# Performance work log

Hardware: AMD Instinct MI355X
Metric: run time of the kernel (lower is better)

## Reference

```python
import jax, jax.numpy as jnp
import numpy as np


def setup_inputs() -> dict:
    key = jax.random.key(0)
    k1, k2 = jax.random.split(key)
    B, D, H, W, K = 64, 256, 32, 32, 1024
    x = jax.random.normal(k1, (B, D, H, W), dtype=jnp.float32)
    # codebook: torch.rand -> uniform [0,1), shape (emb_dim, num_emb)
    emb = jax.random.uniform(k2, (D, K), dtype=jnp.float32)
    return {"x": x, "emb": emb}


def reference(x, emb):
    # x: (B, D, H, W); emb: (D, K)
    B, D, H, W = x.shape
    K = emb.shape[1]
    # flatten latents: (N, D) with N = B*H*W (matches permute(0,2,3,1).view)
    xf = x.transpose(0, 2, 3, 1).reshape(-1, D)
    # (argmin of squared dist == argmin of L2 norm in the torch code)
    d2 = (
        jnp.sum(xf * xf, axis=1, keepdims=True)
        - 2.0 * (xf @ emb)
        + jnp.sum(emb * emb, axis=0)[None, :]
    )  # (N, K)
    argmin = jnp.argmin(d2, axis=1)  # (N,)
    q = jnp.take(emb.T, argmin, axis=0)  # (N, D) gather of nearest codes
    out = q.reshape(B, H, W, D).transpose(0, 3, 1, 2)  # back to (B, D, H, W)
    return out, argmin.reshape(B, H, W)
```

## Files before the change

kernel.cpp:

```cpp
#include <hip/hip_runtime.h>


typedef _Float16 half8 __attribute__((ext_vector_type(8)));
typedef float f32x4v __attribute__((ext_vector_type(4)));
typedef float f32x16 __attribute__((ext_vector_type(16)));
typedef const __attribute__((address_space(1))) unsigned int* gp_t;
typedef __attribute__((address_space(3))) unsigned int* lp_t;

#define K_DIM 1024
#define D_DIM 256

__global__ __launch_bounds__(256) void vq_prep(const float* __restrict__ emb,
                                               float* __restrict__ nhp,
                                               char* __restrict__ eimg_h,
                                               char* __restrict__ eimg_l) {
  __shared__ float tile[32][66];
  const int t = threadIdx.x;
  const int ki = blockIdx.x >> 3, di = blockIdx.x & 7;
  const int d0 = di * 32, k0 = ki * 64;
#pragma unroll
  for (int r = 0; r < 4; ++r) {
    int slot = r * 256 + t;
    int dr = slot >> 5, c2 = slot & 31;
    float2 v = *(const float2*)(emb + (size_t)(d0 + dr) * K_DIM + k0 + c2 * 2);
    *(float2*)&tile[dr][c2 * 2] = v;
  }
  __syncthreads();
  const int codeL = t >> 2, q = t & 3;
  half8 hh, ll;
  float s = 0.f;
#pragma unroll
  for (int j = 0; j < 8; ++j) {
    float v = tile[q * 8 + j][codeL];
    _Float16 h = (_Float16)v;
    hh[j] = h;
    ll[j] = (_Float16)(v - (float)h);
    s = fmaf(v, v, s);
  }
  const int dblk = di * 4 + q;
  const int phys = dblk ^ (codeL & 31);
  const size_t off = (size_t)ki * 32768 + codeL * 512 + phys * 16;
  *(half8*)(eimg_h + off) = hh;
  *(half8*)(eimg_l + off) = ll;
  s += __shfl_xor(s, 1);
  s += __shfl_xor(s, 2);
  if (q == 0) nhp[di * K_DIM + k0 + codeL] = s;
}

#define STAGE(tile_i, bufsel)                                                \
  {                                                                          \
    const size_t tb = (size_t)(tile_i) * 32768 + w * 1024 + l * 16;          \
    _Pragma("unroll") for (int r = 0; r < 8; ++r) {                          \
      __builtin_amdgcn_global_load_lds((gp_t)(eimg_h + tb + r * 4096),       \
                                       (lp_t)(ebuf_h[bufsel] + w * 1024 +    \
                                              r * 4096),                     \
                                       16, 0, 0);                            \
      __builtin_amdgcn_global_load_lds((gp_t)(eimg_l + tb + r * 4096),       \
                                       (lp_t)(ebuf_l[bufsel] + w * 1024 +    \
                                              r * 4096),                     \
                                       16, 0, 0);                            \
    }                                                                        \
  }

__global__ __launch_bounds__(256, 1) void vq_main(
    const float* __restrict__ x, const float* __restrict__ emb,
    const float* __restrict__ nhp, const char* __restrict__ eimg_h,
    const char* __restrict__ eimg_l, float* __restrict__ out,
    float* __restrict__ aout) {
  __shared__ __align__(16) char ebuf_h[2][32768];
  __shared__ __align__(16) char ebuf_l[2][32768];
  __shared__ __align__(16) float x_lds[16][256];
  __shared__ float nh_s[1024];
  __shared__ int bk_s[256];

  const int t = threadIdx.x;
  const int w = t >> 6, l = t & 63, lr = l & 31, lhi = l >> 5;
  const int b = blockIdx.x >> 2;
  const int hw0 = (blockIdx.x & 3) * 256;
  const float* xb = x + (size_t)b * D_DIM * K_DIM + hw0;

#pragma unroll
  for (int i = 0; i < 4; ++i) {
    int c = i * 256 + t;
    float s = 0.f;
#pragma unroll
    for (int p = 0; p < 8; ++p) s += nhp[p * K_DIM + c];
    nh_s[c] = 0.5f * s;
  }

  STAGE(0, 0);

  half8 Bh[2][16], Bl[2][16];
  for (int c = 0; c < 16; ++c) {
    __syncthreads();
#pragma unroll
    for (int i = 0; i < 4; ++i) {
      int slot = i * 256 + t;
      int dr = slot >> 6, c4 = slot & 63;
      float4 v = *(const float4*)(xb + (size_t)(c * 16 + dr) * K_DIM + c4 * 4);
      *(float4*)&x_lds[dr][c4 * 4] = v;
    }
    __syncthreads();
#pragma unroll
    for (int Nt = 0; Nt < 2; ++Nt) {
      int row = w * 64 + Nt * 32 + lr;
      half8 hv, lv;
#pragma unroll
      for (int j = 0; j < 8; ++j) {
        float v = x_lds[lhi * 8 + j][row];
        _Float16 h = (_Float16)v;
        hv[j] = h;
        lv[j] = (_Float16)(v - (float)h);
      }
      Bh[Nt][c] = hv;
      Bl[Nt][c] = lv;
    }
  }

  float bestv[2] = {-3.4e38f, -3.4e38f};
  int bestk[2] = {0, 0};

  for (int ti = 0; ti < 16; ++ti) {
    const int buf = ti & 1;
    if (ti < 15) STAGE(ti + 1, buf ^ 1);
    f32x16 acc[2][2];
#pragma unroll
    for (int Mt = 0; Mt < 2; ++Mt)
#pragma unroll
      for (int rg = 0; rg < 4; ++rg) {
        f32x4v nv = *(const f32x4v*)&nh_s[ti * 64 + Mt * 32 + rg * 8 + lhi * 4];
#pragma unroll
        for (int j = 0; j < 4; ++j) {
          acc[Mt][0][rg * 4 + j] = -nv[j];
          acc[Mt][1][rg * 4 + j] = -nv[j];
        }
      }
#pragma unroll
    for (int ks = 0; ks < 16; ++ks) {
      const int po = ((ks * 2 + lhi) ^ lr) * 16;
      half8 Ah0 = *(const half8*)(ebuf_h[buf] + lr * 512 + po);
      half8 Ah1 = *(const half8*)(ebuf_h[buf] + 16384 + lr * 512 + po);
      half8 Al0 = *(const half8*)(ebuf_l[buf] + lr * 512 + po);
      half8 Al1 = *(const half8*)(ebuf_l[buf] + 16384 + lr * 512 + po);
#pragma unroll
      for (int Nt = 0; Nt < 2; ++Nt) {
        acc[0][Nt] = __builtin_amdgcn_mfma_f32_32x32x16_f16(Ah0, Bh[Nt][ks],
                                                            acc[0][Nt], 0, 0, 0);
        acc[1][Nt] = __builtin_amdgcn_mfma_f32_32x32x16_f16(Ah1, Bh[Nt][ks],
                                                            acc[1][Nt], 0, 0, 0);
      }
#pragma unroll
      for (int Nt = 0; Nt < 2; ++Nt) {
        acc[0][Nt] = __builtin_amdgcn_mfma_f32_32x32x16_f16(Al0, Bh[Nt][ks],
                                                            acc[0][Nt], 0, 0, 0);
        acc[1][Nt] = __builtin_amdgcn_mfma_f32_32x32x16_f16(Al1, Bh[Nt][ks],
                                                            acc[1][Nt], 0, 0, 0);
      }
#pragma unroll
      for (int Nt = 0; Nt < 2; ++Nt) {
        acc[0][Nt] = __builtin_amdgcn_mfma_f32_32x32x16_f16(Ah0, Bl[Nt][ks],
                                                            acc[0][Nt], 0, 0, 0);
        acc[1][Nt] = __builtin_amdgcn_mfma_f32_32x32x16_f16(Ah1, Bl[Nt][ks],
                                                            acc[1][Nt], 0, 0, 0);
      }
    }
#pragma unroll
    for (int Mt = 0; Mt < 2; ++Mt)
#pragma unroll
      for (int reg = 0; reg < 16; ++reg) {
        int code = ti * 64 + Mt * 32 + (reg & 3) + 8 * (reg >> 2) + 4 * lhi;
#pragma unroll
        for (int Nt = 0; Nt < 2; ++Nt) {
          float v = acc[Mt][Nt][reg];
          if (v > bestv[Nt] || (v == bestv[Nt] && code < bestk[Nt])) {
            bestv[Nt] = v;
            bestk[Nt] = code;
          }
        }
      }
    __syncthreads();
  }

#pragma unroll
  for (int Nt = 0; Nt < 2; ++Nt) {
    float v = bestv[Nt];
    int k = bestk[Nt];
    float ov = __shfl_xor(v, 32);
    int ok = __shfl_xor(k, 32);
    if (ov > v || (ov == v && ok < k)) { v = ov; k = ok; }
    if (lhi == 0) {
      int row = w * 64 + Nt * 32 + lr;
      bk_s[row] = k;
      aout[(size_t)blockIdx.x * 256 + row] = (float)k;
    }
  }
  __syncthreads();
  int kk0 = bk_s[l * 4], kk1 = bk_s[l * 4 + 1], kk2 = bk_s[l * 4 + 2],
      kk3 = bk_s[l * 4 + 3];
#pragma unroll 4
  for (int i = 0; i < 64; ++i) {
    int d = w * 64 + i;
    const float* er = emb + (size_t)d * K_DIM;
    float4 v = {er[kk0], er[kk1], er[kk2], er[kk3]};
    *(float4*)(out + ((size_t)b * D_DIM + d) * K_DIM + hw0 + l * 4) = v;
  }
}

extern "C" void kernel_launch(void* const* d_in, const int* in_sizes, int n_in,
                              void* d_out, int out_size, void* d_ws,
                              size_t ws_size, hipStream_t stream) {
  const float* x = (const float*)d_in[0];
  const float* emb = (const float*)d_in[1];
  float* out = (float*)d_out;
  float* aout = out + (size_t)64 * 256 * 32 * 32;
  float* nhp = (float*)d_ws;
  char* eimg_h = (char*)d_ws + 32768;
  char* eimg_l = eimg_h + 524288;
  vq_prep<<<128, 256, 0, stream>>>(emb, nhp, eimg_h, eimg_l);
  vq_main<<<256, 256, 0, stream>>>(x, emb, nhp, eimg_h, eimg_l, out, aout);
}
```

Before: 229.5 us.

## Double block to 512 threads, one N-tile per wave, async x staging

The main kernel now runs 512 threads per block, with each wave owning a single 32-row N tile instead of two. The codebook tiles are therefore staged by twice as many threads with fewer loads each. The x tile is now loaded into double-buffered LDS through async global_load_lds, and the negation of the norms is folded into the precompute. MFMA bursts are wrapped in s_setprio, and the gather/store epilogue is spread across 8 waves. The aim is more waves for latency hiding and lower register pressure per wave, at the cost of each wave reloading the A fragments from LDS for half the work, which increases LDS read traffic.

```diff
diff --git a/kernel.cpp b/kernel.cpp
--- a/kernel.cpp
+++ b/kernel.cpp
@@ -47,29 +47,34 @@
   if (q == 0) nhp[di * K_DIM + k0 + codeL] = s;
 }
 
-#define STAGE(tile_i, bufsel)                                                \
-  {                                                                          \
-    const size_t tb = (size_t)(tile_i) * 32768 + w * 1024 + l * 16;          \
-    _Pragma("unroll") for (int r = 0; r < 8; ++r) {                          \
-      __builtin_amdgcn_global_load_lds((gp_t)(eimg_h + tb + r * 4096),       \
-                                       (lp_t)(ebuf_h[bufsel] + w * 1024 +    \
-                                              r * 4096),                     \
-                                       16, 0, 0);                            \
-      __builtin_amdgcn_global_load_lds((gp_t)(eimg_l + tb + r * 4096),       \
-                                       (lp_t)(ebuf_l[bufsel] + w * 1024 +    \
-                                              r * 4096),                     \
-                                       16, 0, 0);                            \
-    }                                                                        \
-  }
-
-__global__ __launch_bounds__(256, 1) void vq_main(
+#define STAGE(tile_i, bufsel)                                                 \
+  {                                                                           \
+    const size_t tb = (size_t)(tile_i) * 32768 + t * 16;                      \
+    _Pragma("unroll") for (int r = 0; r < 4; ++r) {                           \
+      __builtin_amdgcn_global_load_lds((gp_t)(eimg_h + tb + r * 8192),        \
+                                       (lp_t)(ebuf_h[bufsel] + t * 16 +       \
+                                              r * 8192),                      \
+                                       16, 0, 0);                             \
+      __builtin_amdgcn_global_load_lds((gp_t)(eimg_l + tb + r * 8192),        \
+                                       (lp_t)(ebuf_l[bufsel] + t * 16 +       \
+                                              r * 8192),                      \
+                                       16, 0, 0);                             \
+    }                                                                         \
+  }
+
+#define XSTAGE(ci, xb_sel)                                                    \
+  __builtin_amdgcn_global_load_lds(                                           \
+      (gp_t)(xb + (size_t)((ci) * 8 + (t >> 6)) * K_DIM + (t & 63) * 4),      \
+      (lp_t)((char*)x_lds + (xb_sel) * 8192 + t * 16), 16, 0, 0)
+
+__global__ __launch_bounds__(512, 2) void vq_main(
     const float* __restrict__ x, const float* __restrict__ emb,
     const float* __restrict__ nhp, const char* __restrict__ eimg_h,
     const char* __restrict__ eimg_l, float* __restrict__ out,
     float* __restrict__ aout) {
   __shared__ __align__(16) char ebuf_h[2][32768];
   __shared__ __align__(16) char ebuf_l[2][32768];
-  __shared__ __align__(16) float x_lds[16][256];
+  __shared__ __align__(16) float x_lds[2][8][256];
   __shared__ float nh_s[1024];
   __shared__ int bk_s[256];
 
@@ -78,62 +83,54 @@
   const int b = blockIdx.x >> 2;
   const int hw0 = (blockIdx.x & 3) * 256;
   const float* xb = x + (size_t)b * D_DIM * K_DIM + hw0;
-
-#pragma unroll
-  for (int i = 0; i < 4; ++i) {
-    int c = i * 256 + t;
+  const int myrow = w * 32 + lr;
+
+#pragma unroll
+  for (int i = 0; i < 2; ++i) {
+    int c = i * 512 + t;
     float s = 0.f;
 #pragma unroll
     for (int p = 0; p < 8; ++p) s += nhp[p * K_DIM + c];
-    nh_s[c] = 0.5f * s;
+    nh_s[c] = -0.5f * s;
   }
 
   STAGE(0, 0);
-
-  half8 Bh[2][16], Bl[2][16];
-  for (int c = 0; c < 16; ++c) {
+  XSTAGE(0, 0);
+
+  half8 Bh[16], Bl[16];
+#pragma unroll
+  for (int ci = 0; ci < 32; ++ci) {
     __syncthreads();
-#pragma unroll
-    for (int i = 0; i < 4; ++i) {
-      int slot = i * 256 + t;
-      int dr = slot >> 6, c4 = slot & 63;
-      float4 v = *(const float4*)(xb + (size_t)(c * 16 + dr) * K_DIM + c4 * 4);
-      *(float4*)&x_lds[dr][c4 * 4] = v;
-    }
-    __syncthreads();
-#pragma unroll
-    for (int Nt = 0; Nt < 2; ++Nt) {
-      int row = w * 64 + Nt * 32 + lr;
+    if (ci < 31) XSTAGE(ci + 1, (ci + 1) & 1);
+    if (lhi == (ci & 1)) {
+      const int ks = ci >> 1;
       half8 hv, lv;
 #pragma unroll
       for (int j = 0; j < 8; ++j) {
-        float v = x_lds[lhi * 8 + j][row];
+        float v = x_lds[ci & 1][j][myrow];
         _Float16 h = (_Float16)v;
         hv[j] = h;
         lv[j] = (_Float16)(v - (float)h);
       }
-      Bh[Nt][c] = hv;
-      Bl[Nt][c] = lv;
-    }
-  }
-
-  float bestv[2] = {-3.4e38f, -3.4e38f};
-  int bestk[2] = {0, 0};
+      Bh[ks] = hv;
+      Bl[ks] = lv;
+    }
+  }
+
+  float bestv = -3.4e38f;
+  int bestk = 0;
 
   for (int ti = 0; ti < 16; ++ti) {
     const int buf = ti & 1;
     if (ti < 15) STAGE(ti + 1, buf ^ 1);
-    f32x16 acc[2][2];
+    f32x16 acc[2];
 #pragma unroll
     for (int Mt = 0; Mt < 2; ++Mt)
 #pragma unroll
       for (int rg = 0; rg < 4; ++rg) {
         f32x4v nv = *(const f32x4v*)&nh_s[ti * 64 + Mt * 32 + rg * 8 + lhi * 4];
 #pragma unroll
-        for (int j = 0; j < 4; ++j) {
-          acc[Mt][0][rg * 4 + j] = -nv[j];
-          acc[Mt][1][rg * 4 + j] = -nv[j];
-        }
+        for (int j = 0; j < 4; ++j) acc[Mt][rg * 4 + j] = nv[j];
       }
 #pragma unroll
     for (int ks = 0; ks < 16; ++ks) {
@@ -142,67 +139,51 @@
       half8 Ah1 = *(const half8*)(ebuf_h[buf] + 16384 + lr * 512 + po);
       half8 Al0 = *(const half8*)(ebuf_l[buf] + lr * 512 + po);
       half8 Al1 = *(const half8*)(ebuf_l[buf] + 16384 + lr * 512 + po);
-#pragma unroll
-      for (int Nt = 0; Nt < 2; ++Nt) {
-        acc[0][Nt] = __builtin_amdgcn_mfma_f32_32x32x16_f16(Ah0, Bh[Nt][ks],
-                                                            acc[0][Nt], 0, 0, 0);
-        acc[1][Nt] = __builtin_amdgcn_mfma_f32_32x32x16_f16(Ah1, Bh[Nt][ks],
-                                                            acc[1][Nt], 0, 0, 0);
-      }
-#pragma unroll
-      for (int Nt = 0; Nt < 2; ++Nt) {
-        acc[0][Nt] = __builtin_amdgcn_mfma_f32_32x32x16_f16(Al0, Bh[Nt][ks],
-                                                            acc[0][Nt], 0, 0, 0);
-        acc[1][Nt] = __builtin_amdgcn_mfma_f32_32x32x16_f16(Al1, Bh[Nt][ks],
-                                                            acc[1][Nt], 0, 0, 0);
-      }
-#pragma unroll
-      for (int Nt = 0; Nt < 2; ++Nt) {
-        acc[0][Nt] = __builtin_amdgcn_mfma_f32_32x32x16_f16(Ah0, Bl[Nt][ks],
-                                                            acc[0][Nt], 0, 0, 0);
-        acc[1][Nt] = __builtin_amdgcn_mfma_f32_32x32x16_f16(Ah1, Bl[Nt][ks],
-                                                            acc[1][Nt], 0, 0, 0);
-      }
+      __builtin_amdgcn_s_setprio(1);
+      acc[0] = __builtin_amdgcn_mfma_f32_32x32x16_f16(Ah0, Bh[ks], acc[0], 0, 0, 0);
+      acc[1] = __builtin_amdgcn_mfma_f32_32x32x16_f16(Ah1, Bh[ks], acc[1], 0, 0, 0);
+      acc[0] = __builtin_amdgcn_mfma_f32_32x32x16_f16(Al0, Bh[ks], acc[0], 0, 0, 0);
+      acc[1] = __builtin_amdgcn_mfma_f32_32x32x16_f16(Al1, Bh[ks], acc[1], 0, 0, 0);
+      acc[0] = __builtin_amdgcn_mfma_f32_32x32x16_f16(Ah0, Bl[ks], acc[0], 0, 0, 0);
+      acc[1] = __builtin_amdgcn_mfma_f32_32x32x16_f16(Ah1, Bl[ks], acc[1], 0, 0, 0);
+      __builtin_amdgcn_s_setprio(0);
     }
 #pragma unroll
     for (int Mt = 0; Mt < 2; ++Mt)
 #pragma unroll
       for (int reg = 0; reg < 16; ++reg) {
         int code = ti * 64 + Mt * 32 + (reg & 3) + 8 * (reg >> 2) + 4 * lhi;
-#pragma unroll
-        for (int Nt = 0; Nt < 2; ++Nt) {
-          float v = acc[Mt][Nt][reg];
-          if (v > bestv[Nt] || (v == bestv[Nt] && code < bestk[Nt])) {
-            bestv[Nt] = v;
-            bestk[Nt] = code;
-          }
+        float v = acc[Mt][reg];
+        if (v > bestv || (v == bestv && code < bestk)) {
+          bestv = v;
+          bestk = code;
         }
       }
     __syncthreads();
   }
 
-#pragma unroll
-  for (int Nt = 0; Nt < 2; ++Nt) {
-    float v = bestv[Nt];
-    int k = bestk[Nt];
-    float ov = __shfl_xor(v, 32);
-    int ok = __shfl_xor(k, 32);
-    if (ov > v || (ov == v && ok < k)) { v = ov; k = ok; }
+  {
+    float ov = __shfl_xor(bestv, 32);
+    int ok = __shfl_xor(bestk, 32);
+    if (ov > bestv || (ov == bestv && ok < bestk)) {
+      bestv = ov;
+      bestk = ok;
+    }
     if (lhi == 0) {
-      int row = w * 64 + Nt * 32 + lr;
-      bk_s[row] = k;
-      aout[(size_t)blockIdx.x * 256 + row] = (float)k;
+      bk_s[myrow] = bestk;
+      aout[(size_t)blockIdx.x * 256 + myrow] = (float)bestk;
     }
   }
   __syncthreads();
-  int kk0 = bk_s[l * 4], kk1 = bk_s[l * 4 + 1], kk2 = bk_s[l * 4 + 2],
-      kk3 = bk_s[l * 4 + 3];
+  const int dgrp = t >> 6, n4 = (t & 63) * 4;
+  const int kk0 = bk_s[n4], kk1 = bk_s[n4 + 1], kk2 = bk_s[n4 + 2],
+            kk3 = bk_s[n4 + 3];
 #pragma unroll 4
-  for (int i = 0; i < 64; ++i) {
-    int d = w * 64 + i;
+  for (int i = 0; i < 32; ++i) {
+    int d = i * 8 + dgrp;
     const float* er = emb + (size_t)d * K_DIM;
     float4 v = {er[kk0], er[kk1], er[kk2], er[kk3]};
-    *(float4*)(out + ((size_t)b * D_DIM + d) * K_DIM + hw0 + l * 4) = v;
+    *(float4*)(out + ((size_t)b * D_DIM + d) * K_DIM + hw0 + n4) = v;
   }
 }
 
@@ -217,5 +198,5 @@
   char* eimg_h = (char*)d_ws + 32768;
   char* eimg_l = eimg_h + 524288;
   vq_prep<<<128, 256, 0, stream>>>(emb, nhp, eimg_h, eimg_l);
-  vq_main<<<256, 256, 0, stream>>>(x, emb, nhp, eimg_h, eimg_l, out, aout);
+  vq_main<<<256, 512, 0, stream>>>(x, emb, nhp, eimg_h, eimg_l, out, aout);
 }
```

After: 235.0 us. 2.4% more time.
